# Kernel tuning notes

Hardware: AMD Instinct MI355X
Metric: run time of the kernel (lower is better)

## Reference

```python
import jax, jax.numpy as jnp
import numpy as np

# split_shape from init_kwargs: list of (K, L) = (num slices, slice length)
SPLITS = [(1, 400), (60, 256), (36, 256)]
D_MODEL = 512
BATCH = 2048
EPS = 1e-5  # torch LayerNorm default


def setup_inputs() -> dict:
    key = jax.random.key(0)
    n = len(SPLITS)
    ks = jax.random.split(key, 1 + n)
    total_dim = sum(k * l for k, l in SPLITS)
    inp = {"x": jax.random.normal(ks[0], (BATCH, total_dim), jnp.float32)}
    for i, (k, l) in enumerate(SPLITS):
        # orthogonal-ish init approximated by scaled normal; LN affine = identity
        inp[f"W{i}"] = jax.random.normal(ks[1 + i], (l, D_MODEL), jnp.float32) / np.sqrt(l).astype(np.float32)
        inp[f"b{i}"] = jnp.zeros((D_MODEL,), jnp.float32)
        inp[f"g{i}"] = jnp.ones((D_MODEL,), jnp.float32)
        inp[f"be{i}"] = jnp.zeros((D_MODEL,), jnp.float32)
    return inp


def _fc_block(xs, W, b, g, be):
    # xs: [B, K, L] -> Linear + ReLU + LayerNorm -> [B, K, D]
    h = jax.nn.relu(jnp.einsum('bkl,ld->bkd', xs, W) + b)
    mu = jnp.mean(h, axis=-1, keepdims=True)
    var = jnp.var(h, axis=-1, keepdims=True)
    return (h - mu) * jax.lax.rsqrt(var + EPS) * g + be


def reference(x, W0, b0, g0, be0, W1, b1, g1, be1, W2, b2, g2, be2):
    params = [(W0, b0, g0, be0), (W1, b1, g1, be1), (W2, b2, g2, be2)]
    outs = []
    start = 0
    B = x.shape[0]
    for (k, l), (W, b, g, be) in zip(SPLITS, params):
        # the torch loop over j (K slices) is one batched GEMM after a reshape
        seg = x[:, start:start + k * l].reshape(B, k, l)
        outs.append(_fc_block(seg, W, b, g, be))
        start += k * l
    # torch.stack(x1, 1) over all K_i slices == concat of per-split [B,K_i,D]
    return jnp.concatenate(outs, axis=1)  # [B, sum(K_i)=97, D]
```

## Files before the change

kernel.cpp:

```cpp
#include <hip/hip_runtime.h>

#define TOTAL_DIM 24976
#define N_ROWS    97
#define D_MODEL   512
#define EPSLN     1e-5f

#define NB0 64
#define NB1 3840
#define NB2 2304

#define WT_TOTAL 475136
#define WT_BYTES (WT_TOTAL * 2)

typedef __attribute__((ext_vector_type(8))) short frag8;
typedef __attribute__((ext_vector_type(4))) float frag4;

__device__ __forceinline__ unsigned short f2b(float f) {
  unsigned u = __float_as_uint(f);
  u = u + 0x7fffu + ((u >> 16) & 1u);
  return (unsigned short)(u >> 16);
}

__device__ __forceinline__ void async_copy16(const void* g, void* l) {
  __builtin_amdgcn_global_load_lds(
      (const __attribute__((address_space(1))) void*)g,
      (__attribute__((address_space(3))) void*)l, 16, 0, 0);
}

__global__ void __launch_bounds__(256) prep_wt(const float* __restrict__ W0,
                                               const float* __restrict__ W1,
                                               const float* __restrict__ W2,
                                               unsigned short* __restrict__ wt) {
  int i = blockIdx.x * 256 + threadIdx.x;
  if (i < 212992) {
    int n = i / 416, kp = i - n * 416;
    float v = (kp < 400) ? W0[kp * 512 + n] : 0.f;
    wt[i] = f2b(v);
  } else if (i < 344064) {
    int j = i - 212992;
    int n = j >> 8, kp = j & 255;
    wt[i] = f2b(W1[kp * 512 + n]);
  } else if (i < WT_TOTAL) {
    int j = i - 344064;
    int n = j >> 8, kp = j & 255;
    wt[i] = f2b(W2[kp * 512 + n]);
  }
}

template <int S>
__device__ __forceinline__ void run_split(
    int blk, char* smem,
    const float* __restrict__ x, const unsigned short* __restrict__ wt,
    const float* __restrict__ bias, const float* __restrict__ gam,
    const float* __restrict__ bet, float* __restrict__ out) {
  constexpr int L     = (S == 0) ? 400 : 256;
  constexpr int KP    = (S == 0) ? 416 : 256;
  constexpr int START = (S == 0) ? 0 : (S == 1) ? 400 : 15760;
  constexpr int KK    = (S == 0) ? 1 : (S == 1) ? 60 : 36;
  constexpr int OFF   = (S == 0) ? 0 : (S == 1) ? 1 : 61;
  constexpr int WTO   = (S == 0) ? 0 : (S == 1) ? 212992 : 344064;
  constexpr int NSTEP = KP / 32;

  unsigned short* Blds = (unsigned short*)smem;
  unsigned short* Alds = (unsigned short*)(smem + 32768);
  float* red  = (float*)(smem + 35328);
  float* stat = (float*)(smem + 36352);

  const int tid  = threadIdx.x;
  const int lane = tid & 63, wave = tid >> 6;
  const int q = lane >> 4, c = lane & 15;
  const int m_base = blk * 32;

  const int arow = tid >> 3;
  const int akq  = (tid & 7) * 4;
  const float* aptr;
  {
    int m = m_base + arow;
    int bb = m / KK, jj = m - bb * KK;
    aptr = x + (size_t)bb * TOTAL_DIM + START + jj * L + akq;
  }

  const unsigned short* bptr[8];
  unsigned short* bdst[8];
#pragma unroll
  for (int r = 0; r < 8; ++r) {
    int p = r * 256 + tid;
    int n = p >> 2;
    int kc = ((p & 3) ^ ((n >> 1) & 3)) * 8;
    bptr[r] = wt + WTO + n * KP + kc;
    bdst[r] = Blds + (size_t)(r * 256 + wave * 64) * 8;
  }

  const int a_off0 = (c) * 40 + q * 8;
  const int a_off1 = (16 + c) * 40 + q * 8;
  int b_off[8];
#pragma unroll
  for (int nt = 0; nt < 8; ++nt) {
    int n = wave * 128 + nt * 16 + c;
    b_off[nt] = (n * 4 + (q ^ ((n >> 1) & 3))) * 8;
  }

  frag4 acc[2][8];
#pragma unroll
  for (int mt = 0; mt < 2; ++mt)
#pragma unroll
    for (int nt = 0; nt < 8; ++nt) {
      frag4 z = {0.f, 0.f, 0.f, 0.f};
      acc[mt][nt] = z;
    }

  for (int t = 0; t < NSTEP; ++t) {
#pragma unroll
    for (int r = 0; r < 8; ++r) async_copy16(bptr[r], bdst[r]);

    float4 av;
    const float* p = aptr + t * 32;
    if (S == 0) {
      int k = t * 32 + akq;
      av.x = (k + 0 < L) ? p[0] : 0.f;
      av.y = (k + 1 < L) ? p[1] : 0.f;
      av.z = (k + 2 < L) ? p[2] : 0.f;
      av.w = (k + 3 < L) ? p[3] : 0.f;
    } else {
      av = *(const float4*)p;
    }
    unsigned lo = (unsigned)f2b(av.x) | ((unsigned)f2b(av.y) << 16);
    unsigned hi = (unsigned)f2b(av.z) | ((unsigned)f2b(av.w) << 16);
    *(uint2*)(Alds + arow * 40 + akq) = make_uint2(lo, hi);

#pragma unroll
    for (int r = 0; r < 8; ++r) bptr[r] += 32;

    __syncthreads();

    frag8 a0 = *(const frag8*)(Alds + a_off0);
    frag8 a1 = *(const frag8*)(Alds + a_off1);
#pragma unroll
    for (int nt = 0; nt < 8; ++nt) {
      frag8 bf = *(const frag8*)(Blds + b_off[nt]);
      acc[0][nt] = __builtin_amdgcn_mfma_f32_16x16x32_bf16(a0, bf, acc[0][nt], 0, 0, 0);
      acc[1][nt] = __builtin_amdgcn_mfma_f32_16x16x32_bf16(a1, bf, acc[1][nt], 0, 0, 0);
    }
    __syncthreads();
  }

  const int colbase = wave * 128 + c;
  float bv[8], gv[8], ev[8];
#pragma unroll
  for (int nt = 0; nt < 8; ++nt) {
    int col = colbase + nt * 16;
    bv[nt] = bias[col];
    gv[nt] = gam[col];
    ev[nt] = bet[col];
  }

#pragma unroll
  for (int mt = 0; mt < 2; ++mt) {
    float s[4] = {0.f, 0.f, 0.f, 0.f}, s2[4] = {0.f, 0.f, 0.f, 0.f};
#pragma unroll
    for (int nt = 0; nt < 8; ++nt)
#pragma unroll
      for (int r = 0; r < 4; ++r) {
        float h = acc[mt][nt][r] + bv[nt];
        h = fmaxf(h, 0.f);
        acc[mt][nt][r] = h;
        s[r] += h;
        s2[r] += h * h;
      }
#pragma unroll
    for (int r = 0; r < 4; ++r) {
      float a = s[r], b2 = s2[r];
#pragma unroll
      for (int msk = 1; msk < 16; msk <<= 1) {
        a += __shfl_xor(a, msk, 64);
        b2 += __shfl_xor(b2, msk, 64);
      }
      if (c == 0) {
        int row = mt * 16 + q * 4 + r;
        red[(wave * 32 + row) * 2 + 0] = a;
        red[(wave * 32 + row) * 2 + 1] = b2;
      }
    }
  }
  __syncthreads();
  if (tid < 32) {
    float s = 0.f, s2 = 0.f;
#pragma unroll
    for (int w = 0; w < 4; ++w) {
      s  += red[(w * 32 + tid) * 2 + 0];
      s2 += red[(w * 32 + tid) * 2 + 1];
    }
    float mu  = s * (1.f / 512.f);
    float var = s2 * (1.f / 512.f) - mu * mu;
    stat[tid * 2 + 0] = mu;
    stat[tid * 2 + 1] = rsqrtf(var + EPSLN);
  }
  __syncthreads();

#pragma unroll
  for (int mt = 0; mt < 2; ++mt)
#pragma unroll
    for (int r = 0; r < 4; ++r) {
      int row = mt * 16 + q * 4 + r;
      float mu = stat[row * 2 + 0], sc = stat[row * 2 + 1];
      int m = m_base + row;
      int bb = m / KK, jj = m - bb * KK;
      size_t orow = (size_t)bb * N_ROWS + OFF + jj;
      float* op = out + orow * D_MODEL + colbase;
#pragma unroll
      for (int nt = 0; nt < 8; ++nt)
        op[nt * 16] = (acc[mt][nt][r] - mu) * sc * gv[nt] + ev[nt];
    }
}

__global__ void __launch_bounds__(256, 2) fused_kernel(
    const float* __restrict__ x, const unsigned short* __restrict__ wt,
    const float* __restrict__ b0, const float* __restrict__ g0, const float* __restrict__ e0,
    const float* __restrict__ b1, const float* __restrict__ g1, const float* __restrict__ e1,
    const float* __restrict__ b2, const float* __restrict__ g2, const float* __restrict__ e2,
    float* __restrict__ out) {
  extern __shared__ char smem[];
  int bid = blockIdx.x;
  if (bid < NB0)
    run_split<0>(bid, smem, x, wt, b0, g0, e0, out);
  else if (bid < NB0 + NB1)
    run_split<1>(bid - NB0, smem, x, wt, b1, g1, e1, out);
  else
    run_split<2>(bid - NB0 - NB1, smem, x, wt, b2, g2, e2, out);
}

template <int S>
__global__ void __launch_bounds__(256) fallback_split(
    const float* __restrict__ x, const float* __restrict__ W,
    const float* __restrict__ bias, const float* __restrict__ gam,
    const float* __restrict__ bet, float* __restrict__ out) {
  constexpr int L     = (S == 0) ? 400 : 256;
  constexpr int START = (S == 0) ? 0 : (S == 1) ? 400 : 15760;
  constexpr int KK    = (S == 0) ? 1 : (S == 1) ? 60 : 36;
  constexpr int OFF   = (S == 0) ? 0 : (S == 1) ? 1 : 61;

  __shared__ float xs[400];
  __shared__ float rs[4], rs2[4];

  int m = blockIdx.x;
  int bb = m / KK, jj = m - bb * KK;
  const float* xp = x + (size_t)bb * TOTAL_DIM + START + jj * L;
  for (int k = threadIdx.x; k < L; k += 256) xs[k] = xp[k];
  __syncthreads();

  float h[2];
#pragma unroll
  for (int i = 0; i < 2; ++i) {
    int col = threadIdx.x + i * 256;
    float acc = 0.f;
    for (int k = 0; k < L; ++k) acc += xs[k] * W[k * 512 + col];
    h[i] = fmaxf(acc + bias[col], 0.f);
  }

  float s = h[0] + h[1], s2 = h[0] * h[0] + h[1] * h[1];
#pragma unroll
  for (int msk = 1; msk < 64; msk <<= 1) {
    s  += __shfl_xor(s, msk, 64);
    s2 += __shfl_xor(s2, msk, 64);
  }
  int wave = threadIdx.x >> 6, lane = threadIdx.x & 63;
  if (lane == 0) { rs[wave] = s; rs2[wave] = s2; }
  __syncthreads();
  s  = rs[0] + rs[1] + rs[2] + rs[3];
  s2 = rs2[0] + rs2[1] + rs2[2] + rs2[3];
  float mu  = s * (1.f / 512.f);
  float var = s2 * (1.f / 512.f) - mu * mu;
  float sc  = rsqrtf(var + EPSLN);

  float* op = out + ((size_t)bb * N_ROWS + OFF + jj) * D_MODEL;
#pragma unroll
  for (int i = 0; i < 2; ++i) {
    int col = threadIdx.x + i * 256;
    op[col] = (h[i] - mu) * sc * gam[col] + bet[col];
  }
}

extern "C" void kernel_launch(void* const* d_in, const int* in_sizes, int n_in,
                              void* d_out, int out_size, void* d_ws, size_t ws_size,
                              hipStream_t stream) {
  const float* x  = (const float*)d_in[0];
  const float* W0 = (const float*)d_in[1];
  const float* b0 = (const float*)d_in[2];
  const float* g0 = (const float*)d_in[3];
  const float* e0 = (const float*)d_in[4];
  const float* W1 = (const float*)d_in[5];
  const float* b1 = (const float*)d_in[6];
  const float* g1 = (const float*)d_in[7];
  const float* e1 = (const float*)d_in[8];
  const float* W2 = (const float*)d_in[9];
  const float* b2 = (const float*)d_in[10];
  const float* g2 = (const float*)d_in[11];
  const float* e2 = (const float*)d_in[12];
  float* out = (float*)d_out;

  if (ws_size >= (size_t)WT_BYTES) {
    unsigned short* wt = (unsigned short*)d_ws;
    prep_wt<<<(WT_TOTAL + 255) / 256, 256, 0, stream>>>(W0, W1, W2, wt);
    fused_kernel<<<NB0 + NB1 + NB2, 256, 36608, stream>>>(
        x, wt, b0, g0, e0, b1, g1, e1, b2, g2, e2, out);
  } else {
    fallback_split<0><<<2048,   256, 0, stream>>>(x, W0, b0, g0, e0, out);
    fallback_split<1><<<122880, 256, 0, stream>>>(x, W1, b1, g1, e1, out);
    fallback_split<2><<<73728,  256, 0, stream>>>(x, W2, b2, g2, e2, out);
  }
}
```

Measured before the change: 660.1 us.

## Load MFMA fragments directly from global, drop LDS staging and barriers

The GEMM main loop no longer stages A and B tiles through shared memory with async copies and two barriers per step; each lane loads its bf16 weight fragments and fp32 activation fragments straight from global memory into registers and converts activations with packed bf16 conversion instructions. The weight preparation kernel is rewritten as a shared-memory tiled transpose for coalesced reads and writes, and occupancy is raised to three blocks per CU. This removes LDS traffic and synchronization, but each wave now reads overlapping global data redundantly and relies on caches for reuse. The A loads also use uncoalesced strided rows.

```diff
diff --git a/kernel.cpp b/kernel.cpp
--- a/kernel.cpp
+++ b/kernel.cpp
@@ -21,35 +21,49 @@
   return (unsigned short)(u >> 16);
 }
 
-__device__ __forceinline__ void async_copy16(const void* g, void* l) {
-  __builtin_amdgcn_global_load_lds(
-      (const __attribute__((address_space(1))) void*)g,
-      (__attribute__((address_space(3))) void*)l, 16, 0, 0);
+__device__ __forceinline__ unsigned cvt2bf(float lo, float hi) {
+  unsigned r;
+  asm("v_cvt_pk_bf16_f32 %0, %1, %2" : "=v"(r) : "v"(lo), "v"(hi));
+  return r;
 }
 
 __global__ void __launch_bounds__(256) prep_wt(const float* __restrict__ W0,
                                                const float* __restrict__ W1,
                                                const float* __restrict__ W2,
                                                unsigned short* __restrict__ wt) {
-  int i = blockIdx.x * 256 + threadIdx.x;
-  if (i < 212992) {
-    int n = i / 416, kp = i - n * 416;
-    float v = (kp < 400) ? W0[kp * 512 + n] : 0.f;
-    wt[i] = f2b(v);
-  } else if (i < 344064) {
-    int j = i - 212992;
-    int n = j >> 8, kp = j & 255;
-    wt[i] = f2b(W1[kp * 512 + n]);
-  } else if (i < WT_TOTAL) {
-    int j = i - 344064;
-    int n = j >> 8, kp = j & 255;
-    wt[i] = f2b(W2[kp * 512 + n]);
+  __shared__ float tile[32][33];
+  int bid = blockIdx.x;
+  const float* W;
+  int L, KP, WTO, kt, ntile;
+  if (bid < 208) {
+    W = W0; L = 400; KP = 416; WTO = 0;
+    kt = bid % 13; ntile = bid / 13;
+  } else if (bid < 336) {
+    W = W1; L = 256; KP = 256; WTO = 212992;
+    int b = bid - 208; kt = b & 7; ntile = b >> 3;
+  } else {
+    W = W2; L = 256; KP = 256; WTO = 344064;
+    int b = bid - 336; kt = b & 7; ntile = b >> 3;
+  }
+  const int tx = threadIdx.x & 31, ty = threadIdx.x >> 5;
+#pragma unroll
+  for (int i = 0; i < 4; ++i) {
+    int k = kt * 32 + ty + i * 8;
+    int n = ntile * 32 + tx;
+    tile[ty + i * 8][tx] = (k < L) ? W[k * 512 + n] : 0.f;
+  }
+  __syncthreads();
+#pragma unroll
+  for (int i = 0; i < 4; ++i) {
+    int n  = ntile * 32 + ty + i * 8;
+    int kp = kt * 32 + tx;
+    wt[WTO + n * KP + kp] = f2b(tile[tx][ty + i * 8]);
   }
 }
 
 template <int S>
 __device__ __forceinline__ void run_split(
-    int blk, char* smem,
+    int blk,
     const float* __restrict__ x, const unsigned short* __restrict__ wt,
     const float* __restrict__ bias, const float* __restrict__ gam,
     const float* __restrict__ bet, float* __restrict__ out) {
@@ -61,43 +75,26 @@
   constexpr int WTO   = (S == 0) ? 0 : (S == 1) ? 212992 : 344064;
   constexpr int NSTEP = KP / 32;
 
-  unsigned short* Blds = (unsigned short*)smem;
-  unsigned short* Alds = (unsigned short*)(smem + 32768);
-  float* red  = (float*)(smem + 35328);
-  float* stat = (float*)(smem + 36352);
+  __shared__ float red[4][32][2];
+  __shared__ float stat[32][2];
 
   const int tid  = threadIdx.x;
   const int lane = tid & 63, wave = tid >> 6;
   const int q = lane >> 4, c = lane & 15;
   const int m_base = blk * 32;
 
-  const int arow = tid >> 3;
-  const int akq  = (tid & 7) * 4;
-  const float* aptr;
-  {
-    int m = m_base + arow;
+  const float* ap[2];
+#pragma unroll
+  for (int mt = 0; mt < 2; ++mt) {
+    int m = m_base + mt * 16 + c;
     int bb = m / KK, jj = m - bb * KK;
-    aptr = x + (size_t)bb * TOTAL_DIM + START + jj * L + akq;
-  }
-
-  const unsigned short* bptr[8];
-  unsigned short* bdst[8];
-#pragma unroll
-  for (int r = 0; r < 8; ++r) {
-    int p = r * 256 + tid;
-    int n = p >> 2;
-    int kc = ((p & 3) ^ ((n >> 1) & 3)) * 8;
-    bptr[r] = wt + WTO + n * KP + kc;
-    bdst[r] = Blds + (size_t)(r * 256 + wave * 64) * 8;
-  }
-
-  const int a_off0 = (c) * 40 + q * 8;
-  const int a_off1 = (16 + c) * 40 + q * 8;
-  int b_off[8];
+    ap[mt] = x + (size_t)bb * TOTAL_DIM + START + jj * L + q * 8;
+  }
+  const unsigned short* bp[8];
 #pragma unroll
   for (int nt = 0; nt < 8; ++nt) {
     int n = wave * 128 + nt * 16 + c;
-    b_off[nt] = (n * 4 + (q ^ ((n >> 1) & 3))) * 8;
+    bp[nt] = wt + WTO + n * KP + q * 8;
   }
 
   frag4 acc[2][8];
@@ -110,38 +107,33 @@
     }
 
   for (int t = 0; t < NSTEP; ++t) {
-#pragma unroll
-    for (int r = 0; r < 8; ++r) async_copy16(bptr[r], bdst[r]);
-
-    float4 av;
-    const float* p = aptr + t * 32;
-    if (S == 0) {
-      int k = t * 32 + akq;
-      av.x = (k + 0 < L) ? p[0] : 0.f;
-      av.y = (k + 1 < L) ? p[1] : 0.f;
-      av.z = (k + 2 < L) ? p[2] : 0.f;
-      av.w = (k + 3 < L) ? p[3] : 0.f;
-    } else {
-      av = *(const float4*)p;
-    }
-    unsigned lo = (unsigned)f2b(av.x) | ((unsigned)f2b(av.y) << 16);
-    unsigned hi = (unsigned)f2b(av.z) | ((unsigned)f2b(av.w) << 16);
-    *(uint2*)(Alds + arow * 40 + akq) = make_uint2(lo, hi);
-
-#pragma unroll
-    for (int r = 0; r < 8; ++r) bptr[r] += 32;
-
-    __syncthreads();
-
-    frag8 a0 = *(const frag8*)(Alds + a_off0);
-    frag8 a1 = *(const frag8*)(Alds + a_off1);
+    frag8 bf[8];
+#pragma unroll
+    for (int nt = 0; nt < 8; ++nt)
+      bf[nt] = *(const frag8*)(bp[nt] + t * 32);
+
+    frag8 af[2];
+#pragma unroll
+    for (int mt = 0; mt < 2; ++mt) {
+      union { frag8 f; unsigned u[4]; } ua;
+      if (S == 0 && (t * 32 + q * 8) >= L) {
+        ua.u[0] = 0u; ua.u[1] = 0u; ua.u[2] = 0u; ua.u[3] = 0u;
+      } else {
+        float4 lo = *(const float4*)(ap[mt] + t * 32);
+        float4 hi = *(const float4*)(ap[mt] + t * 32 + 4);
+        ua.u[0] = cvt2bf(lo.x, lo.y);
+        ua.u[1] = cvt2bf(lo.z, lo.w);
+        ua.u[2] = cvt2bf(hi.x, hi.y);
+        ua.u[3] = cvt2bf(hi.z, hi.w);
+      }
+      af[mt] = ua.f;
+    }
+
 #pragma unroll
     for (int nt = 0; nt < 8; ++nt) {
-      frag8 bf = *(const frag8*)(Blds + b_off[nt]);
-      acc[0][nt] = __builtin_amdgcn_mfma_f32_16x16x32_bf16(a0, bf, acc[0][nt], 0, 0, 0);
-      acc[1][nt] = __builtin_amdgcn_mfma_f32_16x16x32_bf16(a1, bf, acc[1][nt], 0, 0, 0);
-    }
-    __syncthreads();
+      acc[0][nt] = __builtin_amdgcn_mfma_f32_16x16x32_bf16(af[0], bf[nt], acc[0][nt], 0, 0, 0);
+      acc[1][nt] = __builtin_amdgcn_mfma_f32_16x16x32_bf16(af[1], bf[nt], acc[1][nt], 0, 0, 0);
+    }
   }
 
   const int colbase = wave * 128 + c;
@@ -177,8 +169,8 @@
       }
       if (c == 0) {
         int row = mt * 16 + q * 4 + r;
-        red[(wave * 32 + row) * 2 + 0] = a;
-        red[(wave * 32 + row) * 2 + 1] = b2;
+        red[wave][row][0] = a;
+        red[wave][row][1] = b2;
       }
     }
   }
@@ -187,13 +179,13 @@
     float s = 0.f, s2 = 0.f;
 #pragma unroll
     for (int w = 0; w < 4; ++w) {
-      s  += red[(w * 32 + tid) * 2 + 0];
-      s2 += red[(w * 32 + tid) * 2 + 1];
+      s  += red[w][tid][0];
+      s2 += red[w][tid][1];
     }
     float mu  = s * (1.f / 512.f);
     float var = s2 * (1.f / 512.f) - mu * mu;
-    stat[tid * 2 + 0] = mu;
-    stat[tid * 2 + 1] = rsqrtf(var + EPSLN);
+    stat[tid][0] = mu;
+    stat[tid][1] = rsqrtf(var + EPSLN);
   }
   __syncthreads();
 
@@ -202,7 +194,7 @@
 #pragma unroll
     for (int r = 0; r < 4; ++r) {
       int row = mt * 16 + q * 4 + r;
-      float mu = stat[row * 2 + 0], sc = stat[row * 2 + 1];
+      float mu = stat[row][0], sc = stat[row][1];
       int m = m_base + row;
       int bb = m / KK, jj = m - bb * KK;
       size_t orow = (size_t)bb * N_ROWS + OFF + jj;
@@ -213,20 +205,19 @@
     }
 }
 
-__global__ void __launch_bounds__(256, 2) fused_kernel(
+__global__ void __launch_bounds__(256, 3) fused_kernel(
     const float* __restrict__ x, const unsigned short* __restrict__ wt,
     const float* __restrict__ b0, const float* __restrict__ g0, const float* __restrict__ e0,
     const float* __restrict__ b1, const float* __restrict__ g1, const float* __restrict__ e1,
     const float* __restrict__ b2, const float* __restrict__ g2, const float* __restrict__ e2,
     float* __restrict__ out) {
-  extern __shared__ char smem[];
   int bid = blockIdx.x;
   if (bid < NB0)
-    run_split<0>(bid, smem, x, wt, b0, g0, e0, out);
+    run_split<0>(bid, x, wt, b0, g0, e0, out);
   else if (bid < NB0 + NB1)
-    run_split<1>(bid - NB0, smem, x, wt, b1, g1, e1, out);
+    run_split<1>(bid - NB0, x, wt, b1, g1, e1, out);
   else
-    run_split<2>(bid - NB0 - NB1, smem, x, wt, b2, g2, e2, out);
+    run_split<2>(bid - NB0 - NB1, x, wt, b2, g2, e2, out);
 }
 
 template <int S>
@@ -300,8 +291,8 @@
 
   if (ws_size >= (size_t)WT_BYTES) {
     unsigned short* wt = (unsigned short*)d_ws;
-    prep_wt<<<(WT_TOTAL + 255) / 256, 256, 0, stream>>>(W0, W1, W2, wt);
-    fused_kernel<<<NB0 + NB1 + NB2, 256, 36608, stream>>>(
+    prep_wt<<<464, 256, 0, stream>>>(W0, W1, W2, wt);
+    fused_kernel<<<NB0 + NB1 + NB2, 256, 0, stream>>>(
         x, wt, b0, g0, e0, b1, g1, e1, b2, g2, e2, out);
   } else {
     fallback_split<0><<<2048,   256, 0, stream>>>(x, W0, b0, g0, e0, out);
```

New measurement: 781.3 us. 18.4% more time.

## Restructure fused GEMM to 64-row tiles with 16 waves and register-streamed weights

Applied to the files above, without the earlier changes.

Blocks grow to 1024 threads with 16 waves, and each block handles 64 rows instead of 32. The whole bf16 A tile for the full K is staged into LDS once, with an XOR swizzle, so the per-K-step barriers go away. Weights are pre-packed into MFMA fragment order and each wave streams its 32-column B slice straight from global memory into registers with one-step prefetch, replacing the LDS staging through async copies. Packed bf16 conversion via v_cvt_pk_bf16_f32 is added, which trades the software round-to-nearest-even for the hardware one. The costs are fewer blocks in flight, more LDS per block, and weight reads repeated by every block from L2.

```diff
diff --git a/kernel.cpp b/kernel.cpp
--- a/kernel.cpp
+++ b/kernel.cpp
@@ -5,12 +5,14 @@
 #define D_MODEL   512
 #define EPSLN     1e-5f
 
-#define NB0 64
-#define NB1 3840
-#define NB2 2304
+#define NB0 32
+#define NB1 1920
+#define NB2 1152
 
 #define WT_TOTAL 475136
 #define WT_BYTES (WT_TOTAL * 2)
+
+#define SMEM_FUSED 61952
 
 typedef __attribute__((ext_vector_type(8))) short frag8;
 typedef __attribute__((ext_vector_type(4))) float frag4;
@@ -21,10 +23,10 @@
   return (unsigned short)(u >> 16);
 }
 
-__device__ __forceinline__ void async_copy16(const void* g, void* l) {
-  __builtin_amdgcn_global_load_lds(
-      (const __attribute__((address_space(1))) void*)g,
-      (__attribute__((address_space(3))) void*)l, 16, 0, 0);
+__device__ __forceinline__ unsigned cvt2bf(float lo, float hi) {
+  unsigned r;
+  asm("v_cvt_pk_bf16_f32 %0, %1, %2" : "=v"(r) : "v"(lo), "v"(hi));
+  return r;
 }
 
 __global__ void __launch_bounds__(256) prep_wt(const float* __restrict__ W0,
@@ -32,19 +34,27 @@
                                                const float* __restrict__ W2,
                                                unsigned short* __restrict__ wt) {
   int i = blockIdx.x * 256 + threadIdx.x;
-  if (i < 212992) {
-    int n = i / 416, kp = i - n * 416;
-    float v = (kp < 400) ? W0[kp * 512 + n] : 0.f;
-    wt[i] = f2b(v);
-  } else if (i < 344064) {
-    int j = i - 212992;
-    int n = j >> 8, kp = j & 255;
-    wt[i] = f2b(W1[kp * 512 + n]);
-  } else if (i < WT_TOTAL) {
-    int j = i - 344064;
-    int n = j >> 8, kp = j & 255;
-    wt[i] = f2b(W2[kp * 512 + n]);
-  }
+  if (i >= WT_TOTAL / 4) return;
+  const float* W; int L, NSTEP, u;
+  if (i < 53248)      { W = W0; L = 400; NSTEP = 13; u = i; }
+  else if (i < 86016) { W = W1; L = 256; NSTEP = 8;  u = i - 53248; }
+  else                { W = W2; L = 256; NSTEP = 8;  u = i - 86016; }
+  int j4 = u & 1;
+  int l  = (u >> 1) & 63;
+  int fi = u >> 7;
+  int t  = fi % NSTEP;
+  int nt = fi / NSTEP;
+  int n  = nt * 16 + (l & 15);
+  int k0 = t * 32 + (l >> 4) * 8 + j4 * 4;
+  float v[4];
+#pragma unroll
+  for (int j = 0; j < 4; ++j) {
+    int k = k0 + j;
+    v[j] = (k < L) ? W[k * 512 + n] : 0.f;
+  }
+  unsigned lo = (unsigned)f2b(v[0]) | ((unsigned)f2b(v[1]) << 16);
+  unsigned hi = (unsigned)f2b(v[2]) | ((unsigned)f2b(v[3]) << 16);
+  ((uint2*)wt)[i] = make_uint2(lo, hi);
 }
 
 template <int S>
@@ -55,99 +65,90 @@
     const float* __restrict__ bet, float* __restrict__ out) {
   constexpr int L     = (S == 0) ? 400 : 256;
   constexpr int KP    = (S == 0) ? 416 : 256;
+  constexpr int NSTEP = KP / 32;
   constexpr int START = (S == 0) ? 0 : (S == 1) ? 400 : 15760;
   constexpr int KK    = (S == 0) ? 1 : (S == 1) ? 60 : 36;
   constexpr int OFF   = (S == 0) ? 0 : (S == 1) ? 1 : 61;
   constexpr int WTO   = (S == 0) ? 0 : (S == 1) ? 212992 : 344064;
-  constexpr int NSTEP = KP / 32;
-
-  unsigned short* Blds = (unsigned short*)smem;
-  unsigned short* Alds = (unsigned short*)(smem + 32768);
-  float* red  = (float*)(smem + 35328);
-  float* stat = (float*)(smem + 36352);
+  constexpr int RS    = KP * 2;
+  constexpr bool SWZ  = (S != 0);
+
+  unsigned short* A = (unsigned short*)smem;
+  float* red  = (float*)(smem + 64 * RS);
+  float* stat = (float*)(smem + 64 * RS + 8192);
 
   const int tid  = threadIdx.x;
-  const int lane = tid & 63, wave = tid >> 6;
+  const int lane = tid & 63, w = tid >> 6;
   const int q = lane >> 4, c = lane & 15;
-  const int m_base = blk * 32;
-
-  const int arow = tid >> 3;
-  const int akq  = (tid & 7) * 4;
-  const float* aptr;
+  const int m_base = blk * 64;
+
+  const unsigned short* bp0 = wt + WTO + (2 * w) * (NSTEP * 512) + lane * 8;
+  const unsigned short* bp1 = bp0 + NSTEP * 512;
+
+  frag8 bc0 = *(const frag8*)bp0;
+  frag8 bc1 = *(const frag8*)bp1;
+
   {
-    int m = m_base + arow;
+    int r = tid >> 4, ch = tid & 15;
+    int m = m_base + r;
     int bb = m / KK, jj = m - bb * KK;
-    aptr = x + (size_t)bb * TOTAL_DIM + START + jj * L + akq;
-  }
-
-  const unsigned short* bptr[8];
-  unsigned short* bdst[8];
-#pragma unroll
-  for (int r = 0; r < 8; ++r) {
-    int p = r * 256 + tid;
-    int n = p >> 2;
-    int kc = ((p & 3) ^ ((n >> 1) & 3)) * 8;
-    bptr[r] = wt + WTO + n * KP + kc;
-    bdst[r] = Blds + (size_t)(r * 256 + wave * 64) * 8;
-  }
-
-  const int a_off0 = (c) * 40 + q * 8;
-  const int a_off1 = (16 + c) * 40 + q * 8;
-  int b_off[8];
-#pragma unroll
-  for (int nt = 0; nt < 8; ++nt) {
-    int n = wave * 128 + nt * 16 + c;
-    b_off[nt] = (n * 4 + (q ^ ((n >> 1) & 3))) * 8;
-  }
-
-  frag4 acc[2][8];
-#pragma unroll
-  for (int mt = 0; mt < 2; ++mt)
-#pragma unroll
-    for (int nt = 0; nt < 8; ++nt) {
+    const float* rp = x + (size_t)bb * TOTAL_DIM + START + (size_t)jj * L;
+    constexpr int NPASS = (S == 0) ? 7 : 4;
+#pragma unroll
+    for (int p = 0; p < NPASS; ++p) {
+      int c4 = ch + p * 16;
+      if (S == 0 && c4 >= 104) continue;
+      float4 v;
+      if (S == 0 && c4 >= 100) {
+        v.x = 0.f; v.y = 0.f; v.z = 0.f; v.w = 0.f;
+      } else {
+        v = *(const float4*)(rp + c4 * 4);
+      }
+      unsigned lo = cvt2bf(v.x, v.y), hi = cvt2bf(v.z, v.w);
+      int off = c4 * 8;
+      if (SWZ) off ^= ((r & 7) << 4);
+      *(uint2*)((char*)A + r * RS + off) = make_uint2(lo, hi);
+    }
+  }
+
+  frag4 acc[4][2];
+#pragma unroll
+  for (int mt = 0; mt < 4; ++mt)
+#pragma unroll
+    for (int nt = 0; nt < 2; ++nt) {
       frag4 z = {0.f, 0.f, 0.f, 0.f};
       acc[mt][nt] = z;
     }
 
+  __syncthreads();
+
+  const int sw = SWZ ? ((c & 7) << 4) : 0;
+
+#pragma unroll
   for (int t = 0; t < NSTEP; ++t) {
-#pragma unroll
-    for (int r = 0; r < 8; ++r) async_copy16(bptr[r], bdst[r]);
-
-    float4 av;
-    const float* p = aptr + t * 32;
-    if (S == 0) {
-      int k = t * 32 + akq;
-      av.x = (k + 0 < L) ? p[0] : 0.f;
-      av.y = (k + 1 < L) ? p[1] : 0.f;
-      av.z = (k + 2 < L) ? p[2] : 0.f;
-      av.w = (k + 3 < L) ? p[3] : 0.f;
-    } else {
-      av = *(const float4*)p;
-    }
-    unsigned lo = (unsigned)f2b(av.x) | ((unsigned)f2b(av.y) << 16);
-    unsigned hi = (unsigned)f2b(av.z) | ((unsigned)f2b(av.w) << 16);
-    *(uint2*)(Alds + arow * 40 + akq) = make_uint2(lo, hi);
-
-#pragma unroll
-    for (int r = 0; r < 8; ++r) bptr[r] += 32;
-
-    __syncthreads();
-
-    frag8 a0 = *(const frag8*)(Alds + a_off0);
-    frag8 a1 = *(const frag8*)(Alds + a_off1);
-#pragma unroll
-    for (int nt = 0; nt < 8; ++nt) {
-      frag8 bf = *(const frag8*)(Blds + b_off[nt]);
-      acc[0][nt] = __builtin_amdgcn_mfma_f32_16x16x32_bf16(a0, bf, acc[0][nt], 0, 0, 0);
-      acc[1][nt] = __builtin_amdgcn_mfma_f32_16x16x32_bf16(a1, bf, acc[1][nt], 0, 0, 0);
-    }
-    __syncthreads();
-  }
-
-  const int colbase = wave * 128 + c;
-  float bv[8], gv[8], ev[8];
-#pragma unroll
-  for (int nt = 0; nt < 8; ++nt) {
+    frag8 bn0, bn1;
+    const bool pre = (t + 1 < NSTEP);
+    if (pre) {
+      bn0 = *(const frag8*)(bp0 + (t + 1) * 512);
+      bn1 = *(const frag8*)(bp1 + (t + 1) * 512);
+    }
+    frag8 af[4];
+    const int off = (t * 64 + q * 16) ^ sw;
+#pragma unroll
+    for (int mt = 0; mt < 4; ++mt)
+      af[mt] = *(const frag8*)((char*)A + (mt * 16 + c) * RS + off);
+#pragma unroll
+    for (int mt = 0; mt < 4; ++mt) {
+      acc[mt][0] = __builtin_amdgcn_mfma_f32_16x16x32_bf16(af[mt], bc0, acc[mt][0], 0, 0, 0);
+      acc[mt][1] = __builtin_amdgcn_mfma_f32_16x16x32_bf16(af[mt], bc1, acc[mt][1], 0, 0, 0);
+    }
+    if (pre) { bc0 = bn0; bc1 = bn1; }
+  }
+
+  const int colbase = w * 32 + c;
+  float bv[2], gv[2], ev[2];
+#pragma unroll
+  for (int nt = 0; nt < 2; ++nt) {
     int col = colbase + nt * 16;
     bv[nt] = bias[col];
     gv[nt] = gam[col];
@@ -155,10 +156,10 @@
   }
 
 #pragma unroll
-  for (int mt = 0; mt < 2; ++mt) {
+  for (int mt = 0; mt < 4; ++mt) {
     float s[4] = {0.f, 0.f, 0.f, 0.f}, s2[4] = {0.f, 0.f, 0.f, 0.f};
 #pragma unroll
-    for (int nt = 0; nt < 8; ++nt)
+    for (int nt = 0; nt < 2; ++nt)
 #pragma unroll
       for (int r = 0; r < 4; ++r) {
         float h = acc[mt][nt][r] + bv[nt];
@@ -177,18 +178,18 @@
       }
       if (c == 0) {
         int row = mt * 16 + q * 4 + r;
-        red[(wave * 32 + row) * 2 + 0] = a;
-        red[(wave * 32 + row) * 2 + 1] = b2;
+        red[(w * 64 + row) * 2 + 0] = a;
+        red[(w * 64 + row) * 2 + 1] = b2;
       }
     }
   }
   __syncthreads();
-  if (tid < 32) {
+  if (tid < 64) {
     float s = 0.f, s2 = 0.f;
 #pragma unroll
-    for (int w = 0; w < 4; ++w) {
-      s  += red[(w * 32 + tid) * 2 + 0];
-      s2 += red[(w * 32 + tid) * 2 + 1];
+    for (int ww = 0; ww < 16; ++ww) {
+      s  += red[(ww * 64 + tid) * 2 + 0];
+      s2 += red[(ww * 64 + tid) * 2 + 1];
     }
     float mu  = s * (1.f / 512.f);
     float var = s2 * (1.f / 512.f) - mu * mu;
@@ -198,7 +199,7 @@
   __syncthreads();
 
 #pragma unroll
-  for (int mt = 0; mt < 2; ++mt)
+  for (int mt = 0; mt < 4; ++mt)
 #pragma unroll
     for (int r = 0; r < 4; ++r) {
       int row = mt * 16 + q * 4 + r;
@@ -208,12 +209,12 @@
       size_t orow = (size_t)bb * N_ROWS + OFF + jj;
       float* op = out + orow * D_MODEL + colbase;
 #pragma unroll
-      for (int nt = 0; nt < 8; ++nt)
+      for (int nt = 0; nt < 2; ++nt)
         op[nt * 16] = (acc[mt][nt][r] - mu) * sc * gv[nt] + ev[nt];
     }
 }
 
-__global__ void __launch_bounds__(256, 2) fused_kernel(
+__global__ void __launch_bounds__(1024, 4) fused_kernel(
     const float* __restrict__ x, const unsigned short* __restrict__ wt,
     const float* __restrict__ b0, const float* __restrict__ g0, const float* __restrict__ e0,
     const float* __restrict__ b1, const float* __restrict__ g1, const float* __restrict__ e1,
@@ -300,8 +301,8 @@
 
   if (ws_size >= (size_t)WT_BYTES) {
     unsigned short* wt = (unsigned short*)d_ws;
-    prep_wt<<<(WT_TOTAL + 255) / 256, 256, 0, stream>>>(W0, W1, W2, wt);
-    fused_kernel<<<NB0 + NB1 + NB2, 256, 36608, stream>>>(
+    prep_wt<<<464, 256, 0, stream>>>(W0, W1, W2, wt);
+    fused_kernel<<<NB0 + NB1 + NB2, 1024, SMEM_FUSED, stream>>>(
         x, wt, b0, g0, e0, b1, g1, e1, b2, g2, e2, out);
   } else {
     fallback_split<0><<<2048,   256, 0, stream>>>(x, W0, b0, g0, e0, out);
```

Result: slower. 681.0 us (+3.2%).
